# Performance work log

Measured on AMD Instinct MI355X. Metric: run time of the kernel, lower is better.

## Reference

```python
import jax, jax.numpy as jnp
import numpy as np

B, T, D, H = 4, 2048, 1024, 16
HD = D // H


def setup_inputs() -> dict:
    key = jax.random.key(0)
    ks = jax.random.split(key, 6)
    s = 0.02
    return {
        "x": jax.random.normal(ks[0], (B, T, D), dtype=jnp.float32),
        "padding_mask": jnp.zeros((B, T), dtype=bool),
        "Wq": jax.random.normal(ks[1], (D, D), dtype=jnp.float32) * s,
        "Wk": jax.random.normal(ks[2], (D, D), dtype=jnp.float32) * s,
        "Wv": jax.random.normal(ks[3], (D, D), dtype=jnp.float32) * s,
        "Wo": jax.random.normal(ks[4], (D, D), dtype=jnp.float32) * s,
        "bo": jax.random.normal(ks[5], (D,), dtype=jnp.float32) * s,
    }


def reference(x, padding_mask, Wq, Wk, Wv, Wo, bo):
    # torch nn.Linear: y = x @ W.T
    b, t, d = x.shape
    q = (x @ Wq.T).reshape(b, t, H, HD).transpose(0, 2, 1, 3)  # [B,H,T,hd]
    k = (x @ Wk.T).reshape(b, t, H, HD).transpose(0, 2, 1, 3)
    v = (x @ Wv.T).reshape(b, t, H, HD).transpose(0, 2, 1, 3)

    scores = jnp.einsum("bhid,bhjd->bhij", q, k) / jnp.sqrt(jnp.float32(HD))
    causal = jnp.tril(jnp.ones((t, t), dtype=bool))  # [T,T]
    neg_inf = jnp.float32(-jnp.inf)
    scores = jnp.where(causal[None, None, :, :], scores, neg_inf)
    scores = jnp.where(padding_mask[:, None, None, :], neg_inf, scores)

    attn = jax.nn.softmax(scores, axis=-1)
    out = jnp.einsum("bhij,bhjd->bhid", attn, v)
    out = out.transpose(0, 2, 1, 3).reshape(b, t, d)
    out = out @ Wo.T + bo
    nonpad = (~padding_mask)[:, :, None].astype(out.dtype)
    return out * nonpad
```

## Files before the change

kernel.cpp:

```cpp
#include <hip/hip_runtime.h>

#define B_ 4
#define T_ 2048
#define D_ 1024
#define H_ 16
#define BT_ (B_ * T_)
#define QSCALE (0.125f * 1.44269504088896f)

typedef unsigned short u16;
typedef __attribute__((ext_vector_type(8))) __bf16 bf16x8;
typedef __attribute__((ext_vector_type(4))) float f32x4;

__device__ __forceinline__ u16 f2bf(float f) {
  unsigned u = __builtin_bit_cast(unsigned, f);
  u += 0x7FFFu + ((u >> 16) & 1u);
  return (u16)(u >> 16);
}

__device__ __forceinline__ void gload16(const void* g, void* l) {
  __builtin_amdgcn_global_load_lds(
      (const __attribute__((address_space(1))) void*)g,
      (__attribute__((address_space(3))) void*)l, 16, 0, 0);
}

__global__ void cvt_bf16(const float* __restrict__ in, u16* __restrict__ out, int n4) {
  int i = blockIdx.x * 256 + threadIdx.x;
  if (i >= n4) return;
  const float4 v = ((const float4*)in)[i];
  ushort4 o;
  o.x = f2bf(v.x); o.y = f2bf(v.y); o.z = f2bf(v.z); o.w = f2bf(v.w);
  ((ushort4*)out)[i] = o;
}

__global__ void pm_flags(const unsigned char* __restrict__ pm, unsigned char* __restrict__ fl) {
  int i = threadIdx.x;
  const unsigned long long* p = (const unsigned long long*)(pm + i * 64);
  unsigned long long acc = 0;
#pragma unroll
  for (int k = 0; k < 8; ++k) acc |= p[k];
  fl[i] = acc ? 1 : 0;
}

template<int MODE>
__global__ __launch_bounds__(256, 2) void gemm_bt(
    const u16* __restrict__ A, const u16* __restrict__ Bw,
    float* __restrict__ Cf, const float* __restrict__ bias,
    const unsigned char* __restrict__ rowmask,
    u16* __restrict__ Cq, u16* __restrict__ Ck, u16* __restrict__ Cvt)
{
  __shared__ __align__(16) u16 sA[128 * 64];
  __shared__ __align__(16) u16 sB[128 * 64];
  const int tid = threadIdx.x;
  const int lane = tid & 63, wave = tid >> 6;
  const int g = lane >> 4, s15 = lane & 15;
  const int bm = blockIdx.x * 128, bn = blockIdx.y * 128;
  const int wr = wave >> 1, wc = wave & 1;

  const int srow = lane >> 3;
  const int scol = ((lane & 7) ^ srow) << 3;

  f32x4 acc[4][4] = {};

  for (int kt = 0; kt < 16; ++kt) {
    __syncthreads();
    const int k0 = kt << 6;
#pragma unroll
    for (int c = 0; c < 4; ++c) {
      const int chunk = c * 4 + wave;
      gload16(A  + (size_t)(bm + chunk * 8 + srow) * 1024 + k0 + scol, (char*)sA + chunk * 1024);
      gload16(Bw + (size_t)(bn + chunk * 8 + srow) * 1024 + k0 + scol, (char*)sB + chunk * 1024);
    }
    __syncthreads();
#pragma unroll
    for (int kk = 0; kk < 2; ++kk) {
      const int cb = ((kk << 6) | (g << 4)) ^ ((s15 & 7) << 4);
      bf16x8 af[4], bf[4];
#pragma unroll
      for (int mm = 0; mm < 4; ++mm)
        af[mm] = *(const bf16x8*)((const char*)sA + (wr * 64 + mm * 16 + s15) * 128 + cb);
#pragma unroll
      for (int nn = 0; nn < 4; ++nn)
        bf[nn] = *(const bf16x8*)((const char*)sB + (wc * 64 + nn * 16 + s15) * 128 + cb);
#pragma unroll
      for (int mm = 0; mm < 4; ++mm)
#pragma unroll
        for (int nn = 0; nn < 4; ++nn)
          acc[mm][nn] = __builtin_amdgcn_mfma_f32_16x16x32_bf16(af[mm], bf[nn], acc[mm][nn], 0, 0, 0);
    }
  }

  if (MODE == 1) {
    const int region = bn >> 10;
    const float a = (region == 0) ? QSCALE : 1.f;
#pragma unroll
    for (int mm = 0; mm < 4; ++mm)
#pragma unroll
      for (int nn = 0; nn < 4; ++nn) {
        const int col = bn + wc * 64 + nn * 16 + s15;
        const int colr = col & 1023;
        const int row0 = bm + wr * 64 + mm * 16 + (g << 2);
        if (region == 2) {
          ushort4 w;
          w.x = f2bf(acc[mm][nn][0]); w.y = f2bf(acc[mm][nn][1]);
          w.z = f2bf(acc[mm][nn][2]); w.w = f2bf(acc[mm][nn][3]);
          *(ushort4*)(Cvt + (size_t)colr * BT_ + row0) = w;
        } else {
          u16* dst = region ? Ck : Cq;
#pragma unroll
          for (int r = 0; r < 4; ++r)
            dst[(size_t)(row0 + r) * 1024 + colr] = f2bf(acc[mm][nn][r] * a);
        }
      }
  } else {
#pragma unroll
    for (int mm = 0; mm < 4; ++mm)
#pragma unroll
      for (int nn = 0; nn < 4; ++nn) {
        const int col = bn + wc * 64 + nn * 16 + s15;
        const int row0 = bm + wr * 64 + mm * 16 + (g << 2);
        const float bv = bias[col];
#pragma unroll
        for (int r = 0; r < 4; ++r) {
          float v = acc[mm][nn][r] + bv;
          v = rowmask[row0 + r] ? 0.f : v;
          Cf[(size_t)(row0 + r) * 1024 + col] = v;
        }
      }
  }
}

__global__ __launch_bounds__(256, 2) void attn_fwd(
    const u16* __restrict__ Q, const u16* __restrict__ K,
    const u16* __restrict__ VT, const unsigned char* __restrict__ pm,
    const unsigned char* __restrict__ tileflag, u16* __restrict__ O)
{
  __shared__ __align__(16) u16 sK[2][64 * 64];
  __shared__ __align__(16) u16 sV[2][64 * 64];
  const int tid = threadIdx.x;
  const int lane = tid & 63, wave = tid >> 6;
  const int g = lane >> 4, s15 = lane & 15;
  const int bh = blockIdx.x, b = bh >> 4, h = bh & 15;
  const int q0 = blockIdx.y * 128;
  const int qw = q0 + wave * 32;
  const size_t tokbase = (size_t)b * T_;

  bf16x8 qf[2][2];
#pragma unroll
  for (int nf = 0; nf < 2; ++nf)
#pragma unroll
    for (int ks = 0; ks < 2; ++ks)
      qf[nf][ks] = *(const bf16x8*)(Q + (tokbase + qw + nf * 16 + s15) * D_ + h * 64 + ks * 32 + g * 8);

  const int srow = lane >> 3;
  const int sc = (lane & 7) ^ srow;
  const u16* Kb0 = K + tokbase * D_ + h * 64 + sc * 8;
  const u16* Vb0 = VT + (size_t)(h * 64) * BT_ + tokbase + sc * 8;

  f32x4 o[2][4] = {};
  float m_[2] = {-1e30f, -1e30f}, l_[2] = {0.f, 0.f};

  const int nt = (q0 >> 6) + 2;

#pragma unroll
  for (int c = 0; c < 2; ++c) {
    const int r8 = (c * 4 + wave) * 8;
    gload16(Kb0 + (size_t)(r8 + srow) * D_,  (char*)(&sK[0][0]) + (c * 4 + wave) * 1024);
    gload16(Vb0 + (size_t)(r8 + srow) * BT_, (char*)(&sV[0][0]) + (c * 4 + wave) * 1024);
  }
  __syncthreads();

  for (int t = 0; t < nt; ++t) {
    const int kv0 = t << 6;
    if (t + 1 < nt) {
      const int nb = (t + 1) & 1;
#pragma unroll
      for (int c = 0; c < 2; ++c) {
        const int r8 = (c * 4 + wave) * 8;
        gload16(Kb0 + (size_t)(kv0 + 64 + r8 + srow) * D_,  (char*)(&sK[nb][0]) + (c * 4 + wave) * 1024);
        gload16(Vb0 + (size_t)(r8 + srow) * BT_ + kv0 + 64, (char*)(&sV[nb][0]) + (c * 4 + wave) * 1024);
      }
    }

    if (kv0 <= qw + 31) {
      const u16* kb_ = &sK[t & 1][0];
      const u16* vb_ = &sV[t & 1][0];

      f32x4 st[4][2] = {};
#pragma unroll
      for (int ks = 0; ks < 2; ++ks) {
        bf16x8 kf[4];
#pragma unroll
        for (int jf = 0; jf < 4; ++jf)
          kf[jf] = *(const bf16x8*)(kb_ + (jf * 16 + s15) * 64 + (((ks * 4 + g) ^ (s15 & 7)) << 3));
#pragma unroll
        for (int jf = 0; jf < 4; ++jf)
#pragma unroll
          for (int nf = 0; nf < 2; ++nf)
            st[jf][nf] = __builtin_amdgcn_mfma_f32_16x16x32_bf16(kf[jf], qf[nf][ks], st[jf][nf], 0, 0, 0);
      }

#pragma unroll
      for (int nf = 0; nf < 2; ++nf) {
        if (kv0 + 63 > qw + nf * 16) {
          const int iq = qw + nf * 16 + s15;
#pragma unroll
          for (int jf = 0; jf < 4; ++jf) {
            const int jb = kv0 + jf * 16 + g * 4;
#pragma unroll
            for (int r = 0; r < 4; ++r)
              if (jb + r > iq) st[jf][nf][r] = -1e30f;
          }
        }
      }
      if (tileflag[b * 32 + t]) {
#pragma unroll
        for (int jf = 0; jf < 4; ++jf) {
          const int jb = kv0 + jf * 16 + g * 4;
          uchar4 p4 = *(const uchar4*)(pm + b * T_ + jb);
          const unsigned char* pr = (const unsigned char*)&p4;
#pragma unroll
          for (int r = 0; r < 4; ++r)
            if (pr[r]) { st[jf][0][r] = -1e30f; st[jf][1][r] = -1e30f; }
        }
      }

      float acorr[2];
#pragma unroll
      for (int nf = 0; nf < 2; ++nf) {
        float tm = -1e30f;
#pragma unroll
        for (int jf = 0; jf < 4; ++jf)
#pragma unroll
          for (int r = 0; r < 4; ++r) tm = fmaxf(tm, st[jf][nf][r]);
        tm = fmaxf(tm, __shfl_xor(tm, 16));
        tm = fmaxf(tm, __shfl_xor(tm, 32));
        const float mn = fmaxf(m_[nf], tm);
        acorr[nf] = __builtin_amdgcn_exp2f(m_[nf] - mn);
        m_[nf] = mn;
        float s = 0.f;
#pragma unroll
        for (int jf = 0; jf < 4; ++jf)
#pragma unroll
          for (int r = 0; r < 4; ++r) {
            const float p = __builtin_amdgcn_exp2f(st[jf][nf][r] - mn);
            st[jf][nf][r] = p;
            s += p;
          }
        s += __shfl_xor(s, 16);
        s += __shfl_xor(s, 32);
        l_[nf] = l_[nf] * acorr[nf] + s;
#pragma unroll
        for (int df = 0; df < 4; ++df) o[nf][df] *= acorr[nf];
      }

#pragma unroll
      for (int kb2 = 0; kb2 < 2; ++kb2) {
        bf16x8 vf[4];
#pragma unroll
        for (int df = 0; df < 4; ++df)
          vf[df] = *(const bf16x8*)(vb_ + (df * 16 + s15) * 64 + (((kb2 * 4 + g) ^ (s15 & 7)) << 3));
#pragma unroll
        for (int nf = 0; nf < 2; ++nf) {
          unsigned w00, w01, w10, w11;
          asm("v_cvt_pk_bf16_f32 %0, %1, %2" : "=v"(w00) : "v"(st[2*kb2][nf][0]),   "v"(st[2*kb2][nf][1]));
          asm("v_cvt_pk_bf16_f32 %0, %1, %2" : "=v"(w01) : "v"(st[2*kb2][nf][2]),   "v"(st[2*kb2][nf][3]));
          asm("v_cvt_pk_bf16_f32 %0, %1, %2" : "=v"(w10) : "v"(st[2*kb2+1][nf][0]), "v"(st[2*kb2+1][nf][1]));
          asm("v_cvt_pk_bf16_f32 %0, %1, %2" : "=v"(w11) : "v"(st[2*kb2+1][nf][2]), "v"(st[2*kb2+1][nf][3]));
          asm("v_permlane32_swap_b32 %0, %1" : "+v"(w00), "+v"(w10));
          asm("v_permlane16_swap_b32 %0, %1" : "+v"(w00), "+v"(w10));
          asm("v_permlane32_swap_b32 %0, %1" : "+v"(w01), "+v"(w11));
          asm("v_permlane16_swap_b32 %0, %1" : "+v"(w01), "+v"(w11));
          union { unsigned u[4]; bf16x8 v; } pf;
          pf.u[0] = w00; pf.u[1] = w01; pf.u[2] = w10; pf.u[3] = w11;
#pragma unroll
          for (int df = 0; df < 4; ++df)
            o[nf][df] = __builtin_amdgcn_mfma_f32_16x16x32_bf16(vf[df], pf.v, o[nf][df], 0, 0, 0);
        }
      }
    }
    __syncthreads();
  }

#pragma unroll
  for (int nf = 0; nf < 2; ++nf) {
    const float inv = 1.f / l_[nf];
    u16* orow = O + (tokbase + qw + nf * 16 + s15) * D_ + h * 64 + g * 4;
#pragma unroll
    for (int df = 0; df < 4; ++df) {
      ushort4 w;
      w.x = f2bf(o[nf][df][0] * inv); w.y = f2bf(o[nf][df][1] * inv);
      w.z = f2bf(o[nf][df][2] * inv); w.w = f2bf(o[nf][df][3] * inv);
      *(ushort4*)(orow + df * 16) = w;
    }
  }
}

extern "C" void kernel_launch(void* const* d_in, const int* in_sizes, int n_in,
                              void* d_out, int out_size, void* d_ws, size_t ws_size,
                              hipStream_t stream)
{
  const float* x  = (const float*)d_in[0];
  const unsigned char* pm = (const unsigned char*)d_in[1];
  const float* Wq = (const float*)d_in[2];
  const float* Wk = (const float*)d_in[3];
  const float* Wv = (const float*)d_in[4];
  const float* Wo = (const float*)d_in[5];
  const float* bo = (const float*)d_in[6];
  float* out = (float*)d_out;

  char* w = (char*)d_ws;
  u16* xb  = (u16*)w; w += (size_t)BT_ * D_ * 2;
  u16* wqb = (u16*)w; w += (size_t)D_ * D_ * 2;
  u16* wkb = (u16*)w; w += (size_t)D_ * D_ * 2;
  u16* wvb = (u16*)w; w += (size_t)D_ * D_ * 2;
  u16* wob = (u16*)w; w += (size_t)D_ * D_ * 2;
  u16* qb  = (u16*)w; w += (size_t)BT_ * D_ * 2;
  u16* kbf = (u16*)w; w += (size_t)BT_ * D_ * 2;
  u16* vt  = (u16*)w; w += (size_t)BT_ * D_ * 2;
  u16* ao  = (u16*)w; w += (size_t)BT_ * D_ * 2;
  unsigned char* flags = (unsigned char*)w; w += 256;

  const int nx4 = BT_ * D_ / 4;
  const int nw4 = D_ * D_ / 4;
  cvt_bf16<<<nx4 / 256, 256, 0, stream>>>(x, xb, nx4);
  cvt_bf16<<<nw4 / 256, 256, 0, stream>>>(Wq, wqb, nw4);
  cvt_bf16<<<nw4 / 256, 256, 0, stream>>>(Wk, wkb, nw4);
  cvt_bf16<<<nw4 / 256, 256, 0, stream>>>(Wv, wvb, nw4);
  cvt_bf16<<<nw4 / 256, 256, 0, stream>>>(Wo, wob, nw4);
  pm_flags<<<1, 128, 0, stream>>>(pm, flags);

  gemm_bt<1><<<dim3(64, 24), 256, 0, stream>>>(xb, wqb, nullptr, nullptr, nullptr, qb, kbf, vt);

  attn_fwd<<<dim3(B_ * H_, T_ / 128), 256, 0, stream>>>(qb, kbf, vt, pm, flags, ao);

  gemm_bt<0><<<dim3(64, 8), 256, 0, stream>>>(ao, wob, out, bo, pm, nullptr, nullptr, nullptr);
}
```

Before: 170.3 us.

## Pair causal query tiles per block with 8 waves and lazy softmax rescale

The attention kernel now runs 512 threads (8 waves of 16 query rows each) and has each block process two 128-row query tiles, jpair and 15-jpair, so causal work is balanced across blocks. The grid shrinks to 8 blocks per head, and K/V tile loads are spread across all 512 threads. The online-softmax rescale is skipped unless the running max rises by more than 8 (in log2 units), and s_setprio wraps the MFMA sections. In exchange, each K/V tile feeds half as many query rows per wave, the grid is smaller, and the deferred rescale can let intermediate exponentials grow up to 2^8.

```diff
diff --git a/kernel.cpp b/kernel.cpp
--- a/kernel.cpp
+++ b/kernel.cpp
@@ -129,7 +129,7 @@
   }
 }
 
-__global__ __launch_bounds__(256, 2) void attn_fwd(
+__global__ __launch_bounds__(512, 4) void attn_fwd(
     const u16* __restrict__ Q, const u16* __restrict__ K,
     const u16* __restrict__ VT, const unsigned char* __restrict__ pm,
     const unsigned char* __restrict__ tileflag, u16* __restrict__ O)
@@ -140,156 +140,142 @@
   const int lane = tid & 63, wave = tid >> 6;
   const int g = lane >> 4, s15 = lane & 15;
   const int bh = blockIdx.x, b = bh >> 4, h = bh & 15;
-  const int q0 = blockIdx.y * 128;
-  const int qw = q0 + wave * 32;
+  const int jpair = blockIdx.y;
   const size_t tokbase = (size_t)b * T_;
 
-  bf16x8 qf[2][2];
-#pragma unroll
-  for (int nf = 0; nf < 2; ++nf)
-#pragma unroll
-    for (int ks = 0; ks < 2; ++ks)
-      qf[nf][ks] = *(const bf16x8*)(Q + (tokbase + qw + nf * 16 + s15) * D_ + h * 64 + ks * 32 + g * 8);
-
-  const int srow = lane >> 3;
-  const int sc = (lane & 7) ^ srow;
+  const int srow = tid >> 3;
+  const int sc = (tid & 7) ^ (srow & 7);
   const u16* Kb0 = K + tokbase * D_ + h * 64 + sc * 8;
   const u16* Vb0 = VT + (size_t)(h * 64) * BT_ + tokbase + sc * 8;
 
-  f32x4 o[2][4] = {};
-  float m_[2] = {-1e30f, -1e30f}, l_[2] = {0.f, 0.f};
-
-  const int nt = (q0 >> 6) + 2;
-
-#pragma unroll
-  for (int c = 0; c < 2; ++c) {
-    const int r8 = (c * 4 + wave) * 8;
-    gload16(Kb0 + (size_t)(r8 + srow) * D_,  (char*)(&sK[0][0]) + (c * 4 + wave) * 1024);
-    gload16(Vb0 + (size_t)(r8 + srow) * BT_, (char*)(&sV[0][0]) + (c * 4 + wave) * 1024);
-  }
-  __syncthreads();
-
-  for (int t = 0; t < nt; ++t) {
-    const int kv0 = t << 6;
-    if (t + 1 < nt) {
-      const int nb = (t + 1) & 1;
-#pragma unroll
-      for (int c = 0; c < 2; ++c) {
-        const int r8 = (c * 4 + wave) * 8;
-        gload16(Kb0 + (size_t)(kv0 + 64 + r8 + srow) * D_,  (char*)(&sK[nb][0]) + (c * 4 + wave) * 1024);
-        gload16(Vb0 + (size_t)(r8 + srow) * BT_ + kv0 + 64, (char*)(&sV[nb][0]) + (c * 4 + wave) * 1024);
+#pragma unroll
+  for (int half = 0; half < 2; ++half) {
+    const int qt = half ? (15 - jpair) : jpair;
+    const int q0 = qt * 128;
+    const int qw = q0 + wave * 16;
+    const int nt = 2 * qt + 2;
+
+    bf16x8 qf[2];
+#pragma unroll
+    for (int ks = 0; ks < 2; ++ks)
+      qf[ks] = *(const bf16x8*)(Q + (tokbase + qw + s15) * D_ + h * 64 + ks * 32 + g * 8);
+
+    f32x4 o[4] = {};
+    float m_ = -1e30f, l_ = 0.f;
+
+    gload16(Kb0 + (size_t)srow * D_,  (char*)(&sK[0][0]) + tid * 16);
+    gload16(Vb0 + (size_t)srow * BT_, (char*)(&sV[0][0]) + tid * 16);
+    __syncthreads();
+
+    for (int t = 0; t < nt; ++t) {
+      const int kv0 = t << 6;
+      if (t + 1 < nt) {
+        const int nb = (t + 1) & 1;
+        gload16(Kb0 + (size_t)(kv0 + 64 + srow) * D_,  (char*)(&sK[nb][0]) + tid * 16);
+        gload16(Vb0 + (size_t)srow * BT_ + kv0 + 64,   (char*)(&sV[nb][0]) + tid * 16);
       }
-    }
-
-    if (kv0 <= qw + 31) {
-      const u16* kb_ = &sK[t & 1][0];
-      const u16* vb_ = &sV[t & 1][0];
-
-      f32x4 st[4][2] = {};
-#pragma unroll
-      for (int ks = 0; ks < 2; ++ks) {
-        bf16x8 kf[4];
-#pragma unroll
-        for (int jf = 0; jf < 4; ++jf)
-          kf[jf] = *(const bf16x8*)(kb_ + (jf * 16 + s15) * 64 + (((ks * 4 + g) ^ (s15 & 7)) << 3));
-#pragma unroll
-        for (int jf = 0; jf < 4; ++jf)
-#pragma unroll
-          for (int nf = 0; nf < 2; ++nf)
-            st[jf][nf] = __builtin_amdgcn_mfma_f32_16x16x32_bf16(kf[jf], qf[nf][ks], st[jf][nf], 0, 0, 0);
-      }
-
-#pragma unroll
-      for (int nf = 0; nf < 2; ++nf) {
-        if (kv0 + 63 > qw + nf * 16) {
-          const int iq = qw + nf * 16 + s15;
+
+      if (kv0 <= qw + 15) {
+        const u16* kb_ = &sK[t & 1][0];
+        const u16* vb_ = &sV[t & 1][0];
+
+        f32x4 st[4] = {};
+#pragma unroll
+        for (int ks = 0; ks < 2; ++ks) {
+          bf16x8 kf[4];
+#pragma unroll
+          for (int jf = 0; jf < 4; ++jf)
+            kf[jf] = *(const bf16x8*)(kb_ + (jf * 16 + s15) * 64 + (((ks * 4 + g) ^ (s15 & 7)) << 3));
+          __builtin_amdgcn_s_setprio(1);
+#pragma unroll
+          for (int jf = 0; jf < 4; ++jf)
+            st[jf] = __builtin_amdgcn_mfma_f32_16x16x32_bf16(kf[jf], qf[ks], st[jf], 0, 0, 0);
+          __builtin_amdgcn_s_setprio(0);
+        }
+
+        if (kv0 + 63 > qw) {
+          const int iq = qw + s15;
 #pragma unroll
           for (int jf = 0; jf < 4; ++jf) {
             const int jb = kv0 + jf * 16 + g * 4;
 #pragma unroll
             for (int r = 0; r < 4; ++r)
-              if (jb + r > iq) st[jf][nf][r] = -1e30f;
+              if (jb + r > iq) st[jf][r] = -1e30f;
           }
         }
-      }
-      if (tileflag[b * 32 + t]) {
-#pragma unroll
-        for (int jf = 0; jf < 4; ++jf) {
-          const int jb = kv0 + jf * 16 + g * 4;
-          uchar4 p4 = *(const uchar4*)(pm + b * T_ + jb);
-          const unsigned char* pr = (const unsigned char*)&p4;
-#pragma unroll
-          for (int r = 0; r < 4; ++r)
-            if (pr[r]) { st[jf][0][r] = -1e30f; st[jf][1][r] = -1e30f; }
-        }
-      }
-
-      float acorr[2];
-#pragma unroll
-      for (int nf = 0; nf < 2; ++nf) {
+        if (tileflag[b * 32 + t]) {
+#pragma unroll
+          for (int jf = 0; jf < 4; ++jf) {
+            const int jb = kv0 + jf * 16 + g * 4;
+            uchar4 p4 = *(const uchar4*)(pm + b * T_ + jb);
+            const unsigned char* pr = (const unsigned char*)&p4;
+#pragma unroll
+            for (int r = 0; r < 4; ++r)
+              if (pr[r]) st[jf][r] = -1e30f;
+          }
+        }
+
         float tm = -1e30f;
 #pragma unroll
         for (int jf = 0; jf < 4; ++jf)
-#pragma unroll
-          for (int r = 0; r < 4; ++r) tm = fmaxf(tm, st[jf][nf][r]);
+          tm = fmaxf(tm, fmaxf(fmaxf(st[jf][0], st[jf][1]), fmaxf(st[jf][2], st[jf][3])));
         tm = fmaxf(tm, __shfl_xor(tm, 16));
         tm = fmaxf(tm, __shfl_xor(tm, 32));
-        const float mn = fmaxf(m_[nf], tm);
-        acorr[nf] = __builtin_amdgcn_exp2f(m_[nf] - mn);
-        m_[nf] = mn;
+        if (!__all(tm <= m_ + 8.f)) {
+          const float mn = fmaxf(m_, tm);
+          const float ac = __builtin_amdgcn_exp2f(m_ - mn);
+          m_ = mn;
+          l_ *= ac;
+#pragma unroll
+          for (int df = 0; df < 4; ++df) o[df] *= ac;
+        }
         float s = 0.f;
 #pragma unroll
         for (int jf = 0; jf < 4; ++jf)
 #pragma unroll
           for (int r = 0; r < 4; ++r) {
-            const float p = __builtin_amdgcn_exp2f(st[jf][nf][r] - mn);
-            st[jf][nf][r] = p;
+            const float p = __builtin_amdgcn_exp2f(st[jf][r] - m_);
+            st[jf][r] = p;
             s += p;
           }
         s += __shfl_xor(s, 16);
         s += __shfl_xor(s, 32);
-        l_[nf] = l_[nf] * acorr[nf] + s;
-#pragma unroll
-        for (int df = 0; df < 4; ++df) o[nf][df] *= acorr[nf];
-      }
-
-#pragma unroll
-      for (int kb2 = 0; kb2 < 2; ++kb2) {
-        bf16x8 vf[4];
-#pragma unroll
-        for (int df = 0; df < 4; ++df)
-          vf[df] = *(const bf16x8*)(vb_ + (df * 16 + s15) * 64 + (((kb2 * 4 + g) ^ (s15 & 7)) << 3));
-#pragma unroll
-        for (int nf = 0; nf < 2; ++nf) {
+        l_ += s;
+
+#pragma unroll
+        for (int kb2 = 0; kb2 < 2; ++kb2) {
+          bf16x8 vf[4];
+#pragma unroll
+          for (int df = 0; df < 4; ++df)
+            vf[df] = *(const bf16x8*)(vb_ + (df * 16 + s15) * 64 + (((kb2 * 4 + g) ^ (s15 & 7)) << 3));
           unsigned w00, w01, w10, w11;
-          asm("v_cvt_pk_bf16_f32 %0, %1, %2" : "=v"(w00) : "v"(st[2*kb2][nf][0]),   "v"(st[2*kb2][nf][1]));
-          asm("v_cvt_pk_bf16_f32 %0, %1, %2" : "=v"(w01) : "v"(st[2*kb2][nf][2]),   "v"(st[2*kb2][nf][3]));
-          asm("v_cvt_pk_bf16_f32 %0, %1, %2" : "=v"(w10) : "v"(st[2*kb2+1][nf][0]), "v"(st[2*kb2+1][nf][1]));
-          asm("v_cvt_pk_bf16_f32 %0, %1, %2" : "=v"(w11) : "v"(st[2*kb2+1][nf][2]), "v"(st[2*kb2+1][nf][3]));
+          asm("v_cvt_pk_bf16_f32 %0, %1, %2" : "=v"(w00) : "v"(st[2*kb2][0]),   "v"(st[2*kb2][1]));
+          asm("v_cvt_pk_bf16_f32 %0, %1, %2" : "=v"(w01) : "v"(st[2*kb2][2]),   "v"(st[2*kb2][3]));
+          asm("v_cvt_pk_bf16_f32 %0, %1, %2" : "=v"(w10) : "v"(st[2*kb2+1][0]), "v"(st[2*kb2+1][1]));
+          asm("v_cvt_pk_bf16_f32 %0, %1, %2" : "=v"(w11) : "v"(st[2*kb2+1][2]), "v"(st[2*kb2+1][3]));
           asm("v_permlane32_swap_b32 %0, %1" : "+v"(w00), "+v"(w10));
           asm("v_permlane16_swap_b32 %0, %1" : "+v"(w00), "+v"(w10));
           asm("v_permlane32_swap_b32 %0, %1" : "+v"(w01), "+v"(w11));
           asm("v_permlane16_swap_b32 %0, %1" : "+v"(w01), "+v"(w11));
           union { unsigned u[4]; bf16x8 v; } pf;
           pf.u[0] = w00; pf.u[1] = w01; pf.u[2] = w10; pf.u[3] = w11;
+          __builtin_amdgcn_s_setprio(1);
 #pragma unroll
           for (int df = 0; df < 4; ++df)
-            o[nf][df] = __builtin_amdgcn_mfma_f32_16x16x32_bf16(vf[df], pf.v, o[nf][df], 0, 0, 0);
+            o[df] = __builtin_amdgcn_mfma_f32_16x16x32_bf16(vf[df], pf.v, o[df], 0, 0, 0);
+          __builtin_amdgcn_s_setprio(0);
         }
       }
+      __syncthreads();
     }
-    __syncthreads();
-  }
-
-#pragma unroll
-  for (int nf = 0; nf < 2; ++nf) {
-    const float inv = 1.f / l_[nf];
-    u16* orow = O + (tokbase + qw + nf * 16 + s15) * D_ + h * 64 + g * 4;
+
+    const float inv = 1.f / l_;
+    u16* orow = O + (tokbase + qw + s15) * D_ + h * 64 + g * 4;
 #pragma unroll
     for (int df = 0; df < 4; ++df) {
       ushort4 w;
-      w.x = f2bf(o[nf][df][0] * inv); w.y = f2bf(o[nf][df][1] * inv);
-      w.z = f2bf(o[nf][df][2] * inv); w.w = f2bf(o[nf][df][3] * inv);
+      w.x = f2bf(o[df][0] * inv); w.y = f2bf(o[df][1] * inv);
+      w.z = f2bf(o[df][2] * inv); w.w = f2bf(o[df][3] * inv);
       *(ushort4*)(orow + df * 16) = w;
     }
   }
@@ -331,7 +317,7 @@
 
   gemm_bt<1><<<dim3(64, 24), 256, 0, stream>>>(xb, wqb, nullptr, nullptr, nullptr, qb, kbf, vt);
 
-  attn_fwd<<<dim3(B_ * H_, T_ / 128), 256, 0, stream>>>(qb, kbf, vt, pm, flags, ao);
+  attn_fwd<<<dim3(B_ * H_, 8), 512, 0, stream>>>(qb, kbf, vt, pm, flags, ao);
 
   gemm_bt<0><<<dim3(64, 8), 256, 0, stream>>>(ao, wob, out, bo, pm, nullptr, nullptr, nullptr);
 }
```

Measured after the change: 159.3 us. 1.07x faster.
